# Performance work log

Measured on AMD Instinct MI355X. Metric: run time of the kernel, lower is better.

The kernel has to match this reference:

```python
import jax, jax.numpy as jnp
import numpy as np

L = 4          # num_layers
D = 512        # d_model
NH = 8         # num_heads
DH = 64        # d_head
DFF = 2048     # d_ff
EPS = 1e-5     # nn.LayerNorm default eps


def _layer_norm(x, g, b):
    m = x.mean(axis=-1, keepdims=True)
    v = ((x - m) ** 2).mean(axis=-1, keepdims=True)
    return (x - m) / jnp.sqrt(v + EPS) * g + b


def setup_inputs() -> dict:
    key = jax.random.key(0)
    ks = jax.random.split(key, 14)
    s = 0.02
    z = jax.random.normal(ks[0], (4, 16, D, 8, 8), dtype=jnp.float32)
    Wq = s * jax.random.normal(ks[1], (L, D, NH * DH), dtype=jnp.float32)
    Wk = s * jax.random.normal(ks[2], (L, D, NH * DH), dtype=jnp.float32)
    Wv = s * jax.random.normal(ks[3], (L, D, NH * DH), dtype=jnp.float32)
    Wo = s * jax.random.normal(ks[4], (L, NH * DH, D), dtype=jnp.float32)
    W1 = s * jax.random.normal(ks[5], (L, D, DFF), dtype=jnp.float32)
    b1 = jnp.zeros((L, DFF), dtype=jnp.float32)
    W2 = s * jax.random.normal(ks[6], (L, DFF, D), dtype=jnp.float32)
    b2 = jnp.zeros((L, D), dtype=jnp.float32)
    ln1_g = jnp.ones((L, D), dtype=jnp.float32)
    ln1_b = jnp.zeros((L, D), dtype=jnp.float32)
    ln2_g = jnp.ones((L, D), dtype=jnp.float32)
    ln2_b = jnp.zeros((L, D), dtype=jnp.float32)
    return {"z": z, "Wq": Wq, "Wk": Wk, "Wv": Wv, "Wo": Wo,
            "W1": W1, "b1": b1, "W2": W2, "b2": b2,
            "ln1_g": ln1_g, "ln1_b": ln1_b, "ln2_g": ln2_g, "ln2_b": ln2_b}


def _forward(z, Wq, Wk, Wv, Wo, W1, b1, W2, b2, ln1_g, ln1_b, ln2_g, ln2_b):
    B, T, Dm, H, W = z.shape
    N = H * W
    Tp = T * N  # T' = t*h*w
    # sinusoidal positional embedding over T' positions
    pos = jnp.arange(Tp, dtype=z.dtype)
    inv_freq = 1.0 / (10000.0 ** (jnp.arange(0, Dm, 2, dtype=z.dtype) / Dm))
    si = pos[:, None] * inv_freq[None, :]                 # (T', D/2)
    pos_emb = jnp.concatenate([jnp.sin(si), jnp.cos(si)], axis=-1)[:, None, :]  # (T',1,D)
    # rearrange 'b t d h w -> (t h w) b d'
    x = jnp.transpose(z, (1, 3, 4, 0, 2)).reshape(Tp, B, Dm)
    x = x + pos_emb
    # block-causal mask at block size N (True = masked)
    blk = jnp.arange(Tp) // N
    mask = blk[None, :] > blk[:, None]                    # (T'_q, T'_k)
    scale = 1.0 / np.sqrt(DH)
    outs = []
    for l in range(L):
        # post-lnorm multi-head attention (LN applied before residual add)
        q = (x @ Wq[l]).reshape(Tp, B, NH, DH)
        k = (x @ Wk[l]).reshape(Tp, B, NH, DH)
        v = (x @ Wv[l]).reshape(Tp, B, NH, DH)
        s = jnp.einsum('ibnd,jbnd->ijbn', q, k) * scale
        s = jnp.where(mask[:, :, None, None], -jnp.inf, s)
        p = jax.nn.softmax(s, axis=1)
        av = jnp.einsum('ijbn,jbnd->ibnd', p, v).reshape(Tp, B, NH * DH)
        attn = _layer_norm(av @ Wo[l], ln1_g[l], ln1_b[l])
        x = attn + x
        ff = _layer_norm(jax.nn.relu(x @ W1[l] + b1[l]) @ W2[l] + b2[l], ln2_g[l], ln2_b[l])
        x = ff + x
        outs.append(x)
    out = jnp.stack(outs, axis=1)                         # (T', L, B, D)
    # rearrange '(t h w) l b d -> b t l d h w'
    out = out.reshape(T, H, W, L, B, Dm)
    return jnp.transpose(out, (4, 0, 3, 5, 1, 2))


def reference(z, Wq, Wk, Wv, Wo, W1, b1, W2, b2, ln1_g, ln1_b, ln2_g, ln2_b):
    return _forward(z, Wq, Wk, Wv, Wo, W1, b1, W2, b2, ln1_g, ln1_b, ln2_g, ln2_b)
```

## Files before the change

kernel.cpp:

```cpp
#include <hip/hip_runtime.h>
#include <hip/hip_bf16.h>
#include <math.h>


#define TP 1024
#define BB 4
#define DD 512
#define DHEAD 64
#define DFF 2048
#define MROWS (TP*BB)
#define EPS 1e-5f
#define CSC 0.18033688011112042f

typedef __attribute__((ext_vector_type(8))) short bf16x8;
typedef __attribute__((ext_vector_type(4))) float f32x4;

__device__ __forceinline__ float b2f(unsigned short u) {
    union { unsigned int i; float f; } z; z.i = ((unsigned int)u) << 16; return z.f;
}
__device__ __forceinline__ unsigned short f2bu(float f) {
    __hip_bfloat16 h = __float2bfloat16(f);
    return *reinterpret_cast<unsigned short*>(&h);
}

#define WAITV0() asm volatile("s_waitcnt vmcnt(0)" ::: "memory")
#define WAITV4() asm volatile("s_waitcnt vmcnt(4)" ::: "memory")
#define WAITV8() asm volatile("s_waitcnt vmcnt(8)" ::: "memory")
#define WAITL0() asm volatile("s_waitcnt lgkmcnt(0)" ::: "memory")
__device__ __forceinline__ void hard_barrier() {
    __builtin_amdgcn_sched_barrier(0);
    __builtin_amdgcn_s_barrier();
    __builtin_amdgcn_sched_barrier(0);
}
__device__ __forceinline__ void waitv_ahead(int ahead) {
    if (ahead == 2) WAITV8();
    else if (ahead == 1) WAITV4();
    else WAITV0();
}
#define GLOAD(gp, lp) __builtin_amdgcn_global_load_lds( \
    (const __attribute__((address_space(1))) void*)(gp), \
    (__attribute__((address_space(3))) void*)(lp), 16, 0, 0)

__device__ __forceinline__ int fsw(int row) { return (row ^ (row >> 2)) & 3; }

__global__ __launch_bounds__(256) void embed_kernel(const float* __restrict__ z,
                                                    float* __restrict__ x,
                                                    __hip_bfloat16* __restrict__ x_bf) {
    __shared__ float tile[64][65];
    const int blk = blockIdx.x;
    const int dc = blk & 7, b = (blk >> 3) & 3, t = blk >> 5;
    const int tid = threadIdx.x;
#pragma unroll
    for (int it = 0; it < 4; ++it) {
        int idx = it * 256 + tid;
        int d_i = idx >> 4, hw4 = (idx & 15) * 4;
        int d = dc * 64 + d_i;
        float4 v = *reinterpret_cast<const float4*>(
            z + ((size_t)((b * 16 + t) * 512 + d)) * 64 + hw4);
        int j = d & 255;
        float freq = expf(-(float)(2 * j) * (9.210340371976184f / 512.0f));
        int i0 = t * 64 + hw4;
#pragma unroll
        for (int e = 0; e < 4; ++e) {
            float si = (float)(i0 + e) * freq;
            float pe = (d < 256) ? sinf(si) : cosf(si);
            tile[d_i][hw4 + e] = ((&v.x)[e]) + pe;
        }
    }
    __syncthreads();
#pragma unroll
    for (int it = 0; it < 4; ++it) {
        int idx = it * 256 + tid;
        int hw_o = idx >> 4, dq = (idx & 15) * 4;
        int row = (t * 64 + hw_o) * 4 + b;
        float4 v = make_float4(tile[dq][hw_o], tile[dq + 1][hw_o],
                               tile[dq + 2][hw_o], tile[dq + 3][hw_o]);
        *reinterpret_cast<float4*>(x + (size_t)row * 512 + dc * 64 + dq) = v;
        ushort4 u;
        u.x = f2bu(v.x); u.y = f2bu(v.y); u.z = f2bu(v.z); u.w = f2bu(v.w);
        *reinterpret_cast<ushort4*>((unsigned short*)x_bf + (size_t)row * 512 + dc * 64 + dq) = u;
    }
}

__global__ __launch_bounds__(256) void wt_convert(
    const float* __restrict__ Wq, const float* __restrict__ Wk,
    const float* __restrict__ Wv, const float* __restrict__ Wo,
    const float* __restrict__ W1, const float* __restrict__ W2,
    __hip_bfloat16* __restrict__ wall) {
    __shared__ float tile[32][33];
    const int l = blockIdx.y;
    __hip_bfloat16* wl = wall + (size_t)l * (4 * 512 * 512 + 2 * 512 * 2048);
    int b = blockIdx.x;
    const float* src; __hip_bfloat16* dst; int R, C, local, cbs;
    if (b < 1024) {
        int m = b >> 8; local = b & 255; R = 512; C = 512; cbs = 4;
        src = ((m == 0) ? Wq : (m == 1) ? Wk : (m == 2) ? Wv : Wo) + (size_t)l * 512 * 512;
        dst = wl + m * 512 * 512;
    } else if (b < 2048) {
        local = b - 1024; R = 512; C = 2048; cbs = 6;
        src = W1 + (size_t)l * 512 * 2048; dst = wl + 4 * 512 * 512;
    } else {
        local = b - 2048; R = 2048; C = 512; cbs = 4;
        src = W2 + (size_t)l * 2048 * 512; dst = wl + 4 * 512 * 512 + 512 * 2048;
    }
    int bx = local & ((1 << cbs) - 1), by = local >> cbs;
    int tx = threadIdx.x & 31, ty = threadIdx.x >> 5;
#pragma unroll
    for (int j = 0; j < 4; ++j)
        tile[ty + j * 8][tx] = src[(size_t)(by * 32 + ty + j * 8) * C + bx * 32 + tx];
    __syncthreads();
#pragma unroll
    for (int j = 0; j < 4; ++j)
        dst[(size_t)(bx * 32 + ty + j * 8) * R + by * 32 + tx] =
            __float2bfloat16(tile[tx][ty + j * 8]);
}

template<bool BIAS, bool RELU, bool OUT_BF16>
__global__ __launch_bounds__(256) void gemm_k(const __hip_bfloat16* __restrict__ A,
                                              const __hip_bfloat16* __restrict__ Bt,
                                              const float* __restrict__ bias,
                                              void* __restrict__ Cout,
                                              int N, int K, int ntx) {
    __shared__ __hip_bfloat16 As[4][128 * 32];
    __shared__ __hip_bfloat16 Bs[4][128 * 32];

    const int lb = blockIdx.x;
    const int wg = (lb & 7) * (gridDim.x >> 3) + (lb >> 3);
    const int m0 = (wg / ntx) * 128;
    const int n0 = (wg % ntx) * 128;

    const int tid  = threadIdx.x;
    const int wave = tid >> 6;
    const int lane = tid & 63;
    const int lr   = lane & 15;
    const int hi   = lane >> 4;
    const int lk   = (hi ^ fsw(lr)) << 3;
    const int wr   = (wave >> 1) * 64;
    const int wc   = (wave & 1) * 64;

    f32x4 acc[4][4];
#pragma unroll
    for (int i = 0; i < 4; ++i)
#pragma unroll
        for (int j = 0; j < 4; ++j) acc[i][j] = (f32x4){0.f, 0.f, 0.f, 0.f};

    const int c0 = tid, c1 = tid + 256;
    const __hip_bfloat16* a0 = A  + (size_t)(m0 + (c0 >> 2)) * K + (((c0 & 3) ^ fsw(c0 >> 2)) << 3);
    const __hip_bfloat16* a1 = A  + (size_t)(m0 + (c1 >> 2)) * K + (((c1 & 3) ^ fsw(c1 >> 2)) << 3);
    const __hip_bfloat16* b0 = Bt + (size_t)(n0 + (c0 >> 2)) * K + (((c0 & 3) ^ fsw(c0 >> 2)) << 3);
    const __hip_bfloat16* b1 = Bt + (size_t)(n0 + (c1 >> 2)) * K + (((c1 & 3) ^ fsw(c1 >> 2)) << 3);
    const int o0 = wave * 512, o1 = 2048 + wave * 512;

    const int nst = K >> 5;
#pragma unroll
    for (int s = 0; s < 3; ++s) {
        GLOAD(a0 + s * 32, &As[s][o0]); GLOAD(a1 + s * 32, &As[s][o1]);
        GLOAD(b0 + s * 32, &Bs[s][o0]); GLOAD(b1 + s * 32, &Bs[s][o1]);
    }

    for (int k = 0; k < nst; ++k) {
        const int ahead = (nst - 1 - k >= 2) ? 2 : (nst - 1 - k);
        waitv_ahead(ahead);
        hard_barrier();
        if (k + 3 < nst) {
            const int kk = (k + 3) << 5, bb = (k + 3) & 3;
            GLOAD(a0 + kk, &As[bb][o0]); GLOAD(a1 + kk, &As[bb][o1]);
            GLOAD(b0 + kk, &Bs[bb][o0]); GLOAD(b1 + kk, &Bs[bb][o1]);
        }
        const int buf = k & 3;
        bf16x8 af[4], bfv[4];
#pragma unroll
        for (int i = 0; i < 4; ++i)
            af[i] = *reinterpret_cast<const bf16x8*>(&As[buf][(size_t)(wr + i * 16 + lr) * 32 + lk]);
#pragma unroll
        for (int j = 0; j < 4; ++j)
            bfv[j] = *reinterpret_cast<const bf16x8*>(&Bs[buf][(size_t)(wc + j * 16 + lr) * 32 + lk]);
        __builtin_amdgcn_s_setprio(1);
#pragma unroll
        for (int i = 0; i < 4; ++i)
#pragma unroll
            for (int j = 0; j < 4; ++j)
                acc[i][j] = __builtin_amdgcn_mfma_f32_16x16x32_bf16(af[i], bfv[j], acc[i][j], 0, 0, 0);
        __builtin_amdgcn_s_setprio(0);
    }

#pragma unroll
    for (int j = 0; j < 4; ++j) {
        int col = n0 + wc + j * 16 + lr;
        float bv = BIAS ? bias[col] : 0.0f;
#pragma unroll
        for (int i = 0; i < 4; ++i) {
            int row = m0 + wr + i * 16 + (hi << 2);
#pragma unroll
            for (int r = 0; r < 4; ++r) {
                float v = acc[i][j][r] + bv;
                if (RELU) v = fmaxf(v, 0.0f);
                if (OUT_BF16)
                    ((unsigned short*)Cout)[(size_t)(row + r) * N + col] = f2bu(v);
                else
                    ((float*)Cout)[(size_t)(row + r) * N + col] = v;
            }
        }
    }
}

template<bool BIAS, bool RELU, bool OUT_BF16>
__device__ __forceinline__ void gemm64_body(const __hip_bfloat16* __restrict__ A,
                                            const __hip_bfloat16* __restrict__ Bt,
                                            const float* __restrict__ bias,
                                            void* __restrict__ Cout, int K,
                                            float scale,
                                            __hip_bfloat16* As, __hip_bfloat16* Bs) {
    const int lb = blockIdx.x;
    const int wg = (lb & 7) * (gridDim.x >> 3) + (lb >> 3);
    const int m0 = (wg >> 3) * 64;
    const int n0 = (wg & 7) * 64;

    const int tid  = threadIdx.x;
    const int wave = tid >> 6;
    const int lane = tid & 63;
    const int lr   = lane & 15;
    const int hi   = lane >> 4;
    const int wr   = (wave >> 1) * 32;
    const int wc   = (wave & 1) * 32;

    f32x4 acc[2][2];
#pragma unroll
    for (int i = 0; i < 2; ++i)
#pragma unroll
        for (int j = 0; j < 2; ++j) acc[i][j] = (f32x4){0.f, 0.f, 0.f, 0.f};

    const int c0 = tid, c1 = tid + 256;
    const __hip_bfloat16* a0 = A  + (size_t)(m0 + (c0 >> 3)) * K + (((c0 & 7) ^ ((c0 >> 3) & 7)) << 3);
    const __hip_bfloat16* a1 = A  + (size_t)(m0 + (c1 >> 3)) * K + (((c1 & 7) ^ ((c1 >> 3) & 7)) << 3);
    const __hip_bfloat16* b0 = Bt + (size_t)(n0 + (c0 >> 3)) * K + (((c0 & 7) ^ ((c0 >> 3) & 7)) << 3);
    const __hip_bfloat16* b1 = Bt + (size_t)(n0 + (c1 >> 3)) * K + (((c1 & 7) ^ ((c1 >> 3) & 7)) << 3);
    const int o0 = wave * 512, o1 = 2048 + wave * 512;

    const int nst = K >> 6;
#pragma unroll
    for (int s = 0; s < 3; ++s) {
        if (s < 3 && s < nst) {
            GLOAD(a0 + s * 64, As + s * 4096 + o0); GLOAD(a1 + s * 64, As + s * 4096 + o1);
            GLOAD(b0 + s * 64, Bs + s * 4096 + o0); GLOAD(b1 + s * 64, Bs + s * 4096 + o1);
        }
    }

    for (int k = 0; k < nst; ++k) {
        const int ahead = (nst - 1 - k >= 2) ? 2 : (nst - 1 - k);
        waitv_ahead(ahead);
        hard_barrier();
        if (k + 3 < nst) {
            const int kk = (k + 3) << 6;
            const int bo = ((k + 3) & 3) * 4096;
            GLOAD(a0 + kk, As + bo + o0); GLOAD(a1 + kk, As + bo + o1);
            GLOAD(b0 + kk, Bs + bo + o0); GLOAD(b1 + kk, Bs + bo + o1);
        }
        const __hip_bfloat16* Ab = As + (k & 3) * 4096;
        const __hip_bfloat16* Bb = Bs + (k & 3) * 4096;
        __builtin_amdgcn_s_setprio(1);
#pragma unroll
        for (int ks = 0; ks < 2; ++ks) {
            bf16x8 af[2], bfv[2];
#pragma unroll
            for (int i = 0; i < 2; ++i) {
                int row = wr + i * 16 + lr;
                af[i] = *reinterpret_cast<const bf16x8*>(
                    &Ab[(size_t)row * 64 + (((ks * 4 + hi) ^ (row & 7)) << 3)]);
            }
#pragma unroll
            for (int j = 0; j < 2; ++j) {
                int row = wc + j * 16 + lr;
                bfv[j] = *reinterpret_cast<const bf16x8*>(
                    &Bb[(size_t)row * 64 + (((ks * 4 + hi) ^ (row & 7)) << 3)]);
            }
#pragma unroll
            for (int i = 0; i < 2; ++i)
#pragma unroll
                for (int j = 0; j < 2; ++j)
                    acc[i][j] = __builtin_amdgcn_mfma_f32_16x16x32_bf16(af[i], bfv[j], acc[i][j], 0, 0, 0);
        }
        __builtin_amdgcn_s_setprio(0);
    }

#pragma unroll
    for (int j = 0; j < 2; ++j) {
        int col = n0 + wc + j * 16 + lr;
        float bv = BIAS ? bias[col] : 0.0f;
#pragma unroll
        for (int i = 0; i < 2; ++i) {
            int row = m0 + wr + i * 16 + (hi << 2);
#pragma unroll
            for (int r = 0; r < 4; ++r) {
                float v = acc[i][j][r] * scale + bv;
                if (RELU) v = fmaxf(v, 0.0f);
                if (OUT_BF16)
                    ((unsigned short*)Cout)[(size_t)(row + r) * 512 + col] = f2bu(v);
                else
                    ((float*)Cout)[(size_t)(row + r) * 512 + col] = v;
            }
        }
    }
}

template<bool BIAS, bool RELU, bool OUT_BF16>
__global__ __launch_bounds__(256) void gemm64_k(const __hip_bfloat16* __restrict__ A,
                                                const __hip_bfloat16* __restrict__ Bt,
                                                const float* __restrict__ bias,
                                                void* __restrict__ Cout, int K) {
    __shared__ __hip_bfloat16 As[4 * 64 * 64];
    __shared__ __hip_bfloat16 Bs[4 * 64 * 64];
    gemm64_body<BIAS, RELU, OUT_BF16>(A, Bt, bias, Cout, K, 1.0f, As, Bs);
}

__global__ __launch_bounds__(256) void gemm_qkv64(const __hip_bfloat16* __restrict__ A,
                                                  const __hip_bfloat16* __restrict__ B0,
                                                  const __hip_bfloat16* __restrict__ B1,
                                                  const __hip_bfloat16* __restrict__ B2,
                                                  __hip_bfloat16* __restrict__ C0,
                                                  __hip_bfloat16* __restrict__ C1,
                                                  __hip_bfloat16* __restrict__ C2) {
    __shared__ __hip_bfloat16 As[4 * 64 * 64];
    __shared__ __hip_bfloat16 Bs[4 * 64 * 64];
    int sel = blockIdx.z;
    const __hip_bfloat16* Bt = (sel == 0) ? B0 : (sel == 1) ? B1 : B2;
    __hip_bfloat16* C = (sel == 0) ? C0 : (sel == 1) ? C1 : C2;
    float scale = (sel == 0) ? CSC : 1.0f;
    gemm64_body<false, false, true>(A, Bt, nullptr, (void*)C, 512, scale, As, Bs);
}

__global__ __launch_bounds__(256) void transpose_v(const unsigned short* __restrict__ v,
                                                   unsigned short* __restrict__ vt) {
    __shared__ unsigned short t[64][72];
    const int kb = blockIdx.x;
    const int bn = blockIdx.y;
    const int b = bn >> 3, n = bn & 7;
    const int tid = threadIdx.x;
#pragma unroll
    for (int it = 0; it < 2; ++it) {
        int c = tid + it * 256;
        int row = c >> 3, d0 = (c & 7) * 8;
        const unsigned short* src =
            v + ((size_t)((kb * 64 + row) * 4 + b)) * 512 + n * 64 + d0;
        bf16x8 xv = *reinterpret_cast<const bf16x8*>(src);
#pragma unroll
        for (int e = 0; e < 8; ++e) t[row][d0 + e] = (unsigned short)xv[e];
    }
    __syncthreads();
#pragma unroll
    for (int it = 0; it < 2; ++it) {
        int c = tid + it * 256;
        int d = c >> 3, k0 = (c & 7) * 8;
        bf16x8 o;
#pragma unroll
        for (int e = 0; e < 8; ++e) o[e] = (short)t[k0 + e][d];
        *reinterpret_cast<bf16x8*>(vt + ((size_t)(bn * 64 + d)) * 1024 + kb * 64 + k0) = o;
    }
}

__device__ __forceinline__ int aswz(int row, int col) {
    return (row * 64 + col) ^ ((row & 7) << 3);
}

__device__ __forceinline__ void stage_tile(const unsigned short* gbase, int stride,
                                           unsigned short* lds, int wave, int tid) {
#pragma unroll
    for (int it = 0; it < 2; ++it) {
        int c = tid + it * 256;
        int row = c >> 3;
        int i = (c & 7) ^ (row & 7);
        const unsigned short* g = gbase + (size_t)row * stride + i * 8;
        __builtin_amdgcn_global_load_lds(
            (const __attribute__((address_space(1))) void*)g,
            (__attribute__((address_space(3))) void*)(lds + it * 2048 + wave * 512),
            16, 0, 0);
    }
}

__global__ __launch_bounds__(256) void attn_mfma(const unsigned short* __restrict__ q,
                                                 const unsigned short* __restrict__ k,
                                                 const unsigned short* __restrict__ vt,
                                                 unsigned short* __restrict__ av) {
    __shared__ unsigned short Qs[64 * 64];
    __shared__ unsigned short Ks[4][64 * 64];
    __shared__ unsigned short Vts[4][64 * 64];
    __shared__ unsigned short Ps[64 * 64];

    const int tid = threadIdx.x;
    const int wave = tid >> 6, lane = tid & 63;
    const int lr = lane & 15, hi = lane >> 4;
    const int wr = wave * 16;

    const int p = blockIdx.x;
    const int xcd = p & 7, idx = p >> 3;
    const int bn = xcd * 4 + (idx & 3);
    const int qb = 15 - (idx >> 2);
    const int b = bn >> 3, n = bn & 7;

    const unsigned short* kcol  = k  + (size_t)b * 512 + n * 64;
    const unsigned short* vtrow = vt + (size_t)(bn * 64) * 1024;

    stage_tile(q + ((size_t)(qb * 64) * 4 + b) * 512 + n * 64, 2048, Qs, wave, tid);
    stage_tile(kcol, 2048, Ks[0], wave, tid);
    stage_tile(vtrow, 1024, Vts[0], wave, tid);
    if (qb >= 1) {
        stage_tile(kcol + (size_t)64 * 2048, 2048, Ks[1], wave, tid);
        stage_tile(vtrow + 64, 1024, Vts[1], wave, tid);
    }
    if (qb >= 2) {
        stage_tile(kcol + (size_t)128 * 2048, 2048, Ks[2], wave, tid);
        stage_tile(vtrow + 128, 1024, Vts[2], wave, tid);
    }

    f32x4 o_acc[4], l_acc;
#pragma unroll
    for (int db = 0; db < 4; ++db) o_acc[db] = (f32x4){0.f, 0.f, 0.f, 0.f};
    l_acc = (f32x4){0.f, 0.f, 0.f, 0.f};

    bf16x8 onesf;
#pragma unroll
    for (int e = 0; e < 8; ++e) onesf[e] = (short)0x3F80;

    bf16x8 qf[2];

    for (int kb = 0; kb <= qb; ++kb) {
        const int ahead = (qb - kb >= 2) ? 2 : (qb - kb);
        waitv_ahead(ahead);
        hard_barrier();
        if (kb + 3 <= qb) {
            stage_tile(kcol + (size_t)(kb + 3) * 64 * 2048, 2048,
                       Ks[(kb + 3) & 3], wave, tid);
            stage_tile(vtrow + (kb + 3) * 64, 1024, Vts[(kb + 3) & 3], wave, tid);
        }
        if (kb == 0) {
#pragma unroll
            for (int ks = 0; ks < 2; ++ks)
                qf[ks] = *reinterpret_cast<const bf16x8*>(
                    (const unsigned short*)Qs + aswz(wr + lr, ks * 32 + hi * 8));
        }
        const unsigned short* Kb = Ks[kb & 3];
        const unsigned short* Vb = Vts[kb & 3];

        f32x4 sf[4];
#pragma unroll
        for (int jb = 0; jb < 4; ++jb) sf[jb] = (f32x4){0.f, 0.f, 0.f, 0.f};
        __builtin_amdgcn_s_setprio(1);
#pragma unroll
        for (int ks = 0; ks < 2; ++ks) {
            bf16x8 a = qf[ks];
#pragma unroll
            for (int jb = 0; jb < 4; ++jb) {
                bf16x8 kf = *reinterpret_cast<const bf16x8*>(
                    Kb + aswz(jb * 16 + lr, ks * 32 + hi * 8));
                sf[jb] = __builtin_amdgcn_mfma_f32_16x16x32_bf16(a, kf, sf[jb], 0, 0, 0);
            }
        }
        __builtin_amdgcn_s_setprio(0);

#pragma unroll
        for (int jb = 0; jb < 4; ++jb)
#pragma unroll
            for (int r = 0; r < 4; ++r) {
                float pe = exp2f(fminf(sf[jb][r], 100.0f));
                Ps[aswz(wr + 4 * hi + r, jb * 16 + lr)] = f2bu(pe);
            }
        WAITL0();
        hard_barrier();

        __builtin_amdgcn_s_setprio(1);
#pragma unroll
        for (int ks = 0; ks < 2; ++ks) {
            bf16x8 pf = *reinterpret_cast<const bf16x8*>(
                (const unsigned short*)Ps + aswz(wr + lr, ks * 32 + hi * 8));
            l_acc = __builtin_amdgcn_mfma_f32_16x16x32_bf16(pf, onesf, l_acc, 0, 0, 0);
#pragma unroll
            for (int db = 0; db < 4; ++db) {
                bf16x8 vf = *reinterpret_cast<const bf16x8*>(
                    Vb + aswz(db * 16 + lr, ks * 32 + hi * 8));
                o_acc[db] = __builtin_amdgcn_mfma_f32_16x16x32_bf16(pf, vf, o_acc[db], 0, 0, 0);
            }
        }
        __builtin_amdgcn_s_setprio(0);
    }

#pragma unroll
    for (int r = 0; r < 4; ++r) {
        float inv = 1.0f / l_acc[r];
        int row = qb * 64 + wr + 4 * hi + r;
#pragma unroll
        for (int db = 0; db < 4; ++db)
            av[((size_t)row * 4 + b) * 512 + n * 64 + db * 16 + lr] =
                f2bu(o_acc[db][r] * inv);
    }
}

__global__ __launch_bounds__(64) void add_ln_kernel(const float* __restrict__ y,
                                                    const float* __restrict__ g,
                                                    const float* __restrict__ bta,
                                                    float* __restrict__ x,
                                                    __hip_bfloat16* __restrict__ x_bf) {
    const int row = blockIdx.x;
    const int tid = threadIdx.x;
    const float* yr = y + (size_t)row * DD;
    float4 v0 = *reinterpret_cast<const float4*>(&yr[tid * 4]);
    float4 v1 = *reinterpret_cast<const float4*>(&yr[256 + tid * 4]);
    float s = v0.x + v0.y + v0.z + v0.w + v1.x + v1.y + v1.z + v1.w;
    float ss = v0.x * v0.x + v0.y * v0.y + v0.z * v0.z + v0.w * v0.w +
               v1.x * v1.x + v1.y * v1.y + v1.z * v1.z + v1.w * v1.w;
#pragma unroll
    for (int off = 32; off; off >>= 1) {
        s  += __shfl_xor(s, off);
        ss += __shfl_xor(ss, off);
    }
    float mean = s * (1.0f / 512.0f);
    float var = ss * (1.0f / 512.0f) - mean * mean;
    float rstd = rsqrtf(var + EPS);

    float* xr = x + (size_t)row * DD;
    float vals[8] = {v0.x, v0.y, v0.z, v0.w, v1.x, v1.y, v1.z, v1.w};
#pragma unroll
    for (int e = 0; e < 8; ++e) {
        int d = (e < 4) ? (tid * 4 + e) : (256 + tid * 4 + (e - 4));
        float nrm = (vals[e] - mean) * rstd * g[d] + bta[d];
        float xo = xr[d] + nrm;
        xr[d] = xo;
        x_bf[(size_t)row * DD + d] = __float2bfloat16(xo);
    }
}

__global__ __launch_bounds__(256) void out_transpose(const float* __restrict__ x,
                                                     float* __restrict__ out, int l) {
    __shared__ float tile[64][65];
    const int blk = blockIdx.x;
    const int dc = blk & 7;
    const int b  = (blk >> 3) & 3;
    const int t  = blk >> 5;
    const int tid = threadIdx.x;
#pragma unroll
    for (int it = 0; it < 4; ++it) {
        int c = tid + it * 256;
        int hw = c >> 4, f4 = c & 15;
        const float* src = x + (size_t)((t * 64 + hw) * 4 + b) * 512 + dc * 64 + f4 * 4;
        float4 v = *reinterpret_cast<const float4*>(src);
        tile[hw][f4 * 4 + 0] = v.x; tile[hw][f4 * 4 + 1] = v.y;
        tile[hw][f4 * 4 + 2] = v.z; tile[hw][f4 * 4 + 3] = v.w;
    }
    __syncthreads();
    size_t ob = (((size_t)(b * 16 + t) * 4 + l) * 512 + dc * 64) * 64;
#pragma unroll
    for (int it = 0; it < 4; ++it) {
        int c = tid + it * 256;
        int d = c >> 4, f4 = c & 15;
        float4 v = make_float4(tile[f4 * 4 + 0][d], tile[f4 * 4 + 1][d],
                               tile[f4 * 4 + 2][d], tile[f4 * 4 + 3][d]);
        *reinterpret_cast<float4*>(out + ob + (size_t)d * 64 + f4 * 4) = v;
    }
}

extern "C" void kernel_launch(void* const* d_in, const int* in_sizes, int n_in,
                              void* d_out, int out_size, void* d_ws, size_t ws_size,
                              hipStream_t stream) {
    const float* z    = (const float*)d_in[0];
    const float* Wq   = (const float*)d_in[1];
    const float* Wk   = (const float*)d_in[2];
    const float* Wv   = (const float*)d_in[3];
    const float* Wo   = (const float*)d_in[4];
    const float* W1   = (const float*)d_in[5];
    const float* b1   = (const float*)d_in[6];
    const float* W2   = (const float*)d_in[7];
    const float* b2   = (const float*)d_in[8];
    const float* ln1g = (const float*)d_in[9];
    const float* ln1b = (const float*)d_in[10];
    const float* ln2g = (const float*)d_in[11];
    const float* ln2b = (const float*)d_in[12];
    float* out = (float*)d_out;

    const size_t MB = 1u << 20;
    char* base = (char*)d_ws;
    float*          x     = (float*)(base);
    __hip_bfloat16* x_bf  = (__hip_bfloat16*)(base + 8  * MB);
    __hip_bfloat16* q_bf  = (__hip_bfloat16*)(base + 12 * MB);
    __hip_bfloat16* k_bf  = (__hip_bfloat16*)(base + 16 * MB);
    __hip_bfloat16* v_bf  = (__hip_bfloat16*)(base + 20 * MB);
    __hip_bfloat16* av_bf = (__hip_bfloat16*)(base + 24 * MB);
    float*          tmp   = (float*)(base + 28 * MB);
    __hip_bfloat16* wall  = (__hip_bfloat16*)(base + 36 * MB);
    __hip_bfloat16* ff1_bf = q_bf;
    unsigned short* vt    = (unsigned short*)tmp;

    const size_t WL = 4 * 512 * 512 + 2 * 512 * 2048;

    embed_kernel<<<512, 256, 0, stream>>>(z, x, x_bf);
    wt_convert<<<dim3(3072, 4), 256, 0, stream>>>(Wq, Wk, Wv, Wo, W1, W2, wall);

    for (int l = 0; l < 4; ++l) {
        __hip_bfloat16* wl  = wall + (size_t)l * WL;
        __hip_bfloat16* wqt = wl;
        __hip_bfloat16* wkt = wqt + 512 * 512;
        __hip_bfloat16* wvt = wkt + 512 * 512;
        __hip_bfloat16* wot = wvt + 512 * 512;
        __hip_bfloat16* w1t = wot + 512 * 512;
        __hip_bfloat16* w2t = w1t + 512 * 2048;

        gemm_qkv64<<<dim3(512, 1, 3), 256, 0, stream>>>(x_bf, wqt, wkt, wvt,
                                                        q_bf, k_bf, v_bf);

        transpose_v<<<dim3(16, 32), 256, 0, stream>>>((const unsigned short*)v_bf, vt);

        attn_mfma<<<512, 256, 0, stream>>>(
            (const unsigned short*)q_bf, (const unsigned short*)k_bf,
            vt, (unsigned short*)av_bf);

        gemm64_k<false, false, false><<<512, 256, 0, stream>>>(
            av_bf, wot, nullptr, (void*)tmp, 512);
        add_ln_kernel<<<MROWS, 64, 0, stream>>>(tmp, ln1g + l * 512, ln1b + l * 512,
                                                x, x_bf);

        gemm_k<true, true, true><<<512, 256, 0, stream>>>(
            x_bf, w1t, b1 + l * 2048, (void*)ff1_bf, 2048, 512, 16);
        gemm64_k<true, false, false><<<512, 256, 0, stream>>>(
            ff1_bf, w2t, b2 + l * 512, (void*)tmp, 2048);
        add_ln_kernel<<<MROWS, 64, 0, stream>>>(tmp, ln2g + l * 512, ln2b + l * 512,
                                                x, x_bf);
        out_transpose<<<512, 256, 0, stream>>>(x, out, l);
    }
}
```

Before: 439.8 us.

## Fuse V transpose into QKV GEMM epilogue and fold output transpose into next launch

The V projection GEMM now writes its tile transposed straight to the vt layout through an LDS staging buffer, which removes the separate transpose_v kernel and the round trip of v_bf through memory. The previous layer's out_transpose work is added as a fourth z-slice of the QKV launch, so it runs alongside the GEMM blocks, and only the last layer keeps a standalone out_transpose. This cuts two launches per layer at the cost of a more complex, heterogeneous kernel. vt moves to its own buffer because tmp is no longer free at that point.

```diff
diff --git a/kernel.cpp b/kernel.cpp
--- a/kernel.cpp
+++ b/kernel.cpp
@@ -204,12 +204,13 @@
     }
 }
 
-template<bool BIAS, bool RELU, bool OUT_BF16>
+template<bool BIAS, bool RELU, int OUTMODE>
 __device__ __forceinline__ void gemm64_body(const __hip_bfloat16* __restrict__ A,
                                             const __hip_bfloat16* __restrict__ Bt,
                                             const float* __restrict__ bias,
-                                            void* __restrict__ Cout, int K,
-                                            float scale,
+                                            void* __restrict__ Cout,
+                                            unsigned short* __restrict__ vtout,
+                                            int K, float scale,
                                             __hip_bfloat16* As, __hip_bfloat16* Bs) {
     const int lb = blockIdx.x;
     const int wg = (lb & 7) * (gridDim.x >> 3) + (lb >> 3);
@@ -240,7 +241,7 @@
     const int nst = K >> 6;
 #pragma unroll
     for (int s = 0; s < 3; ++s) {
-        if (s < 3 && s < nst) {
+        if (s < nst) {
             GLOAD(a0 + s * 64, As + s * 4096 + o0); GLOAD(a1 + s * 64, As + s * 4096 + o1);
             GLOAD(b0 + s * 64, Bs + s * 4096 + o0); GLOAD(b1 + s * 64, Bs + s * 4096 + o1);
         }
@@ -283,6 +284,33 @@
         __builtin_amdgcn_s_setprio(0);
     }
 
+    if (OUTMODE == 2) {
+        hard_barrier();
+        unsigned short* T = (unsigned short*)As;
+        const int TS = 68;
+#pragma unroll
+        for (int j = 0; j < 2; ++j)
+#pragma unroll
+            for (int i = 0; i < 2; ++i)
+#pragma unroll
+                for (int r = 0; r < 4; ++r)
+                    T[(wr + i * 16 + (hi << 2) + r) * TS + wc + j * 16 + lr] =
+                        f2bu(acc[i][j][r]);
+        hard_barrier();
+        const int b = tid >> 6, d = tid & 63;
+        const int n = n0 >> 6, t0 = m0 >> 2;
+        bf16x8 v0, v1;
+#pragma unroll
+        for (int e = 0; e < 8; ++e) {
+            v0[e] = (short)T[((e) * 4 + b) * TS + d];
+            v1[e] = (short)T[((e + 8) * 4 + b) * TS + d];
+        }
+        unsigned short* dst = vtout + ((size_t)((b * 8 + n) * 64 + d)) * 1024 + t0;
+        *reinterpret_cast<bf16x8*>(dst) = v0;
+        *reinterpret_cast<bf16x8*>(dst + 8) = v1;
+        return;
+    }
+
 #pragma unroll
     for (int j = 0; j < 2; ++j) {
         int col = n0 + wc + j * 16 + lr;
@@ -294,7 +322,7 @@
             for (int r = 0; r < 4; ++r) {
                 float v = acc[i][j][r] * scale + bv;
                 if (RELU) v = fmaxf(v, 0.0f);
-                if (OUT_BF16)
+                if (OUTMODE == 1)
                     ((unsigned short*)Cout)[(size_t)(row + r) * 512 + col] = f2bu(v);
                 else
                     ((float*)Cout)[(size_t)(row + r) * 512 + col] = v;
@@ -310,51 +338,55 @@
                                                 void* __restrict__ Cout, int K) {
     __shared__ __hip_bfloat16 As[4 * 64 * 64];
     __shared__ __hip_bfloat16 Bs[4 * 64 * 64];
-    gemm64_body<BIAS, RELU, OUT_BF16>(A, Bt, bias, Cout, K, 1.0f, As, Bs);
-}
-
-__global__ __launch_bounds__(256) void gemm_qkv64(const __hip_bfloat16* __restrict__ A,
-                                                  const __hip_bfloat16* __restrict__ B0,
-                                                  const __hip_bfloat16* __restrict__ B1,
-                                                  const __hip_bfloat16* __restrict__ B2,
-                                                  __hip_bfloat16* __restrict__ C0,
-                                                  __hip_bfloat16* __restrict__ C1,
-                                                  __hip_bfloat16* __restrict__ C2) {
+    gemm64_body<BIAS, RELU, OUT_BF16 ? 1 : 0>(A, Bt, bias, Cout, nullptr, K, 1.0f, As, Bs);
+}
+
+__global__ __launch_bounds__(256) void qkv_out_k(const __hip_bfloat16* __restrict__ A,
+                                                 const __hip_bfloat16* __restrict__ B0,
+                                                 const __hip_bfloat16* __restrict__ B1,
+                                                 const __hip_bfloat16* __restrict__ B2,
+                                                 __hip_bfloat16* __restrict__ C0,
+                                                 __hip_bfloat16* __restrict__ C1,
+                                                 unsigned short* __restrict__ vt,
+                                                 const float* __restrict__ x,
+                                                 float* __restrict__ out, int outl) {
     __shared__ __hip_bfloat16 As[4 * 64 * 64];
     __shared__ __hip_bfloat16 Bs[4 * 64 * 64];
-    int sel = blockIdx.z;
-    const __hip_bfloat16* Bt = (sel == 0) ? B0 : (sel == 1) ? B1 : B2;
-    __hip_bfloat16* C = (sel == 0) ? C0 : (sel == 1) ? C1 : C2;
-    float scale = (sel == 0) ? CSC : 1.0f;
-    gemm64_body<false, false, true>(A, Bt, nullptr, (void*)C, 512, scale, As, Bs);
-}
-
-__global__ __launch_bounds__(256) void transpose_v(const unsigned short* __restrict__ v,
-                                                   unsigned short* __restrict__ vt) {
-    __shared__ unsigned short t[64][72];
-    const int kb = blockIdx.x;
-    const int bn = blockIdx.y;
-    const int b = bn >> 3, n = bn & 7;
-    const int tid = threadIdx.x;
-#pragma unroll
-    for (int it = 0; it < 2; ++it) {
-        int c = tid + it * 256;
-        int row = c >> 3, d0 = (c & 7) * 8;
-        const unsigned short* src =
-            v + ((size_t)((kb * 64 + row) * 4 + b)) * 512 + n * 64 + d0;
-        bf16x8 xv = *reinterpret_cast<const bf16x8*>(src);
-#pragma unroll
-        for (int e = 0; e < 8; ++e) t[row][d0 + e] = (unsigned short)xv[e];
-    }
-    __syncthreads();
-#pragma unroll
-    for (int it = 0; it < 2; ++it) {
-        int c = tid + it * 256;
-        int d = c >> 3, k0 = (c & 7) * 8;
-        bf16x8 o;
-#pragma unroll
-        for (int e = 0; e < 8; ++e) o[e] = (short)t[k0 + e][d];
-        *reinterpret_cast<bf16x8*>(vt + ((size_t)(bn * 64 + d)) * 1024 + kb * 64 + k0) = o;
+    const int sel = blockIdx.z;
+    if (sel == 3) {
+        float (*tile)[65] = reinterpret_cast<float(*)[65]>(As);
+        const int blk = blockIdx.x;
+        const int dc = blk & 7;
+        const int b  = (blk >> 3) & 3;
+        const int t  = blk >> 5;
+        const int tid = threadIdx.x;
+#pragma unroll
+        for (int it = 0; it < 4; ++it) {
+            int c = tid + it * 256;
+            int hw = c >> 4, f4 = c & 15;
+            const float* src = x + (size_t)((t * 64 + hw) * 4 + b) * 512 + dc * 64 + f4 * 4;
+            float4 v = *reinterpret_cast<const float4*>(src);
+            tile[hw][f4 * 4 + 0] = v.x; tile[hw][f4 * 4 + 1] = v.y;
+            tile[hw][f4 * 4 + 2] = v.z; tile[hw][f4 * 4 + 3] = v.w;
+        }
+        __syncthreads();
+        size_t ob = (((size_t)(b * 16 + t) * 4 + outl) * 512 + dc * 64) * 64;
+#pragma unroll
+        for (int it = 0; it < 4; ++it) {
+            int c = tid + it * 256;
+            int d = c >> 4, f4 = c & 15;
+            float4 v = make_float4(tile[f4 * 4 + 0][d], tile[f4 * 4 + 1][d],
+                                   tile[f4 * 4 + 2][d], tile[f4 * 4 + 3][d]);
+            *reinterpret_cast<float4*>(out + ob + (size_t)d * 64 + f4 * 4) = v;
+        }
+        return;
+    }
+    if (sel == 2) {
+        gemm64_body<false, false, 2>(A, B2, nullptr, nullptr, vt, 512, 1.0f, As, Bs);
+    } else if (sel == 1) {
+        gemm64_body<false, false, 1>(A, B1, nullptr, (void*)C1, nullptr, 512, 1.0f, As, Bs);
+    } else {
+        gemm64_body<false, false, 1>(A, B0, nullptr, (void*)C0, nullptr, 512, CSC, As, Bs);
     }
 }
 
@@ -581,12 +613,11 @@
     __hip_bfloat16* x_bf  = (__hip_bfloat16*)(base + 8  * MB);
     __hip_bfloat16* q_bf  = (__hip_bfloat16*)(base + 12 * MB);
     __hip_bfloat16* k_bf  = (__hip_bfloat16*)(base + 16 * MB);
-    __hip_bfloat16* v_bf  = (__hip_bfloat16*)(base + 20 * MB);
     __hip_bfloat16* av_bf = (__hip_bfloat16*)(base + 24 * MB);
     float*          tmp   = (float*)(base + 28 * MB);
     __hip_bfloat16* wall  = (__hip_bfloat16*)(base + 36 * MB);
     __hip_bfloat16* ff1_bf = q_bf;
-    unsigned short* vt    = (unsigned short*)tmp;
+    unsigned short* vt    = (unsigned short*)(base + 20 * MB);
 
     const size_t WL = 4 * 512 * 512 + 2 * 512 * 2048;
 
@@ -602,10 +633,8 @@
         __hip_bfloat16* w1t = wot + 512 * 512;
         __hip_bfloat16* w2t = w1t + 512 * 2048;
 
-        gemm_qkv64<<<dim3(512, 1, 3), 256, 0, stream>>>(x_bf, wqt, wkt, wvt,
-                                                        q_bf, k_bf, v_bf);
-
-        transpose_v<<<dim3(16, 32), 256, 0, stream>>>((const unsigned short*)v_bf, vt);
+        qkv_out_k<<<dim3(512, 1, l == 0 ? 3 : 4), 256, 0, stream>>>(
+            x_bf, wqt, wkt, wvt, q_bf, k_bf, vt, x, out, l - 1);
 
         attn_mfma<<<512, 256, 0, stream>>>(
             (const unsigned short*)q_bf, (const unsigned short*)k_bf,
@@ -622,6 +651,6 @@
             ff1_bf, w2t, b2 + l * 512, (void*)tmp, 2048);
         add_ln_kernel<<<MROWS, 64, 0, stream>>>(tmp, ln2g + l * 512, ln2b + l * 512,
                                                 x, x_bf);
-        out_transpose<<<512, 256, 0, stream>>>(x, out, l);
-    }
-}
+    }
+    out_transpose<<<512, 256, 0, stream>>>(x, out, 3);
+}
```

New measurement: 419.0 us. 1.05x faster.
